# Performance work log

Hardware: AMD Instinct MI355X
Metric: run time of the kernel (lower is better)

## Reference

```python
import jax, jax.numpy as jnp
import numpy as np

N, C, H, W = 64, 512, 32, 32
HID, NCLS = 240, 10


def setup_inputs() -> dict:
    key = jax.random.key(0)
    ks = jax.random.split(key, 6)
    d = {
        "x": jax.random.normal(ks[0], (N, C, H, W), jnp.float32),
        "bn1_g": jnp.ones((C,), jnp.float32),
        "bn1_b": jnp.zeros((C,), jnp.float32),
        "bn1_m": jnp.zeros((C,), jnp.float32),
        "bn1_v": jnp.ones((C,), jnp.float32),
        "conv1_w": jax.random.normal(ks[1], (C, C, 3, 3), jnp.float32) * 0.02,
        "bn2_g": jnp.ones((C,), jnp.float32),
        "bn2_b": jnp.zeros((C,), jnp.float32),
        "bn2_m": jnp.zeros((C,), jnp.float32),
        "bn2_v": jnp.ones((C,), jnp.float32),
        "conv2_w": jax.random.normal(ks[2], (C, C, 3, 3), jnp.float32) * 0.02,
        "fc1_w": jax.random.normal(ks[3], (HID, C), jnp.float32) * 0.05,
        "fc1_b": jnp.zeros((HID,), jnp.float32),
        "fc2_w": jax.random.normal(ks[4], (NCLS, HID), jnp.float32) * 0.05,
        "fc2_b": jnp.zeros((NCLS,), jnp.float32),
    }
    return d


def _bn(x, g, b, m, v, eps=1e-5):
    # eval-mode BatchNorm2d, NCHW
    inv = g / jnp.sqrt(v + eps)
    return x * inv[None, :, None, None] + (b - m * inv)[None, :, None, None]


def _conv3(x, w):
    return jax.lax.conv_general_dilated(
        x, w, window_strides=(1, 1), padding="SAME",
        dimension_numbers=("NCHW", "OIHW", "NCHW"))


def _probe(feat, fc1_w, fc1_b, fc2_w, fc2_b):
    # Global_Avg_Flatten -> Linear -> Softplus(beta=5) -> Linear
    g = feat.mean(axis=(2, 3))                       # (N, C)
    h = jax.nn.softplus(5.0 * (g @ fc1_w.T + fc1_b)) / 5.0  # (N, HID)
    return h @ fc2_w.T + fc2_b                       # (N, NCLS)


def _get_mask(feat, fc1_w, fc1_b, fc2_w, fc2_b):
    # eval branch: sum of top-1 + top-2 logits, grad wrt (detached) feat
    feat_sg = jax.lax.stop_gradient(feat)

    def logit_sum(f_):
        logits = _probe(f_, fc1_w, fc1_b, fc2_w, fc2_b)
        idx = jax.lax.top_k(logits, 2)[1]            # (N, 2) int indices
        return jnp.take_along_axis(logits, idx, axis=1).sum()

    g = jax.grad(logit_sum)(feat_sg)                 # (N, C, H, W)
    # adaptive_avg_pool2d(.,1)*H*W == spatial sum
    s = g.sum(axis=(2, 3))                           # (N, C)
    m = jax.nn.softmax(s, axis=1) * 2.0
    return m[:, :, None, None]


def reference(x, bn1_g, bn1_b, bn1_m, bn1_v, conv1_w,
              bn2_g, bn2_b, bn2_m, bn2_v, conv2_w,
              fc1_w, fc1_b, fc2_w, fc2_b):
    out1 = jax.nn.relu(_bn(x, bn1_g, bn1_b, bn1_m, bn1_v))  # equalInOut path
    mask = _get_mask(out1, fc1_w, fc1_b, fc2_w, fc2_b)
    pred_probe = _probe(out1, fc1_w, fc1_b, fc2_w, fc2_b)
    masked = out1 * mask
    h = jax.nn.relu(_bn(_conv3(masked, conv1_w), bn2_g, bn2_b, bn2_m, bn2_v))
    h = _conv3(h, conv2_w)
    out = x + h
    return (out, pred_probe)
```

## Files before the change

kernel.cpp:

```cpp
#include <hip/hip_runtime.h>
#include <stdint.h>

typedef __bf16 bf16x8 __attribute__((ext_vector_type(8)));
typedef float f32x4v __attribute__((ext_vector_type(4)));

typedef __attribute__((address_space(1))) const void gconst_t;
typedef __attribute__((address_space(3))) void lds_t;

#define GLL16(gp, sp) __builtin_amdgcn_global_load_lds((gconst_t*)(uintptr_t)(gp), (lds_t*)(uintptr_t)(sp), 16, 0, 0)

__device__ __forceinline__ unsigned short f2bf(float f) {
  unsigned int u = __float_as_uint(f);
  u = (u + 0x7FFFu + ((u >> 16) & 1u)) >> 16;
  return (unsigned short)u;
}
__device__ __forceinline__ float bf2f(unsigned int b) {
  return __uint_as_float(b << 16);
}

#define SPP 1156

__global__ __launch_bounds__(512) void bnprep(
    const float* __restrict__ g1, const float* __restrict__ b1,
    const float* __restrict__ m1, const float* __restrict__ v1,
    const float* __restrict__ g2, const float* __restrict__ b2,
    const float* __restrict__ m2, const float* __restrict__ v2,
    float* __restrict__ bnp) {
  int t = threadIdx.x;
  float i1 = g1[t] * rsqrtf(v1[t] + 1e-5f);
  bnp[t] = i1;
  bnp[512 + t] = b1[t] - m1[t] * i1;
  float i2 = g2[t] * rsqrtf(v2[t] + 1e-5f);
  bnp[1024 + t] = i2;
  bnp[1536 + t] = b2[t] - m2[t] * i2;
}

__global__ __launch_bounds__(256) void wtrans(const float* __restrict__ w1, const float* __restrict__ w2,
                                              unsigned short* __restrict__ w1t, unsigned short* __restrict__ w2t) {
  unsigned e = blockIdx.x * 256u + threadIdx.x;
  if (e >= 4718592u) return;
  const float* w = (e < 2359296u) ? w1 : w2;
  unsigned short* o = (e < 2359296u) ? w1t : w2t;
  unsigned r = (e < 2359296u) ? e : (e - 2359296u);
  unsigned ci = r & 511u, co = (r >> 9) & 511u, tt = r >> 18;
  o[r] = f2bf(w[(co * 512u + ci) * 9u + tt]);
}

__global__ __launch_bounds__(256) void bn1_relu_stage(const float* __restrict__ x, const float* __restrict__ bnp,
                                                      unsigned short* __restrict__ Ap, float* __restrict__ partial) {
  int bid = blockIdx.x;
  int n = bid >> 6, ciblk = (bid >> 3) & 7, yblk = bid & 7;
  int ci0 = ciblk * 64, y0 = yblk * 4;
  int t = threadIdx.x;
  __shared__ __align__(16) float vals[64 * 128];
  __shared__ float ivs[64], bbs[64];
  if (t < 64) { ivs[t] = bnp[ci0 + t]; bbs[t] = bnp[512 + ci0 + t]; }
  __syncthreads();
#pragma unroll
  for (int i = 0; i < 8; ++i) {
    int f4 = i * 256 + t;
    int cil = f4 >> 5, xq = f4 & 31;
    const float* src = x + ((size_t)(n * 512 + ci0 + cil)) * 1024 + y0 * 32 + xq * 4;
    f32x4v v = *(const f32x4v*)src;
    float iv = ivs[cil], bb = bbs[cil];
    f32x4v r;
    r[0] = fmaxf(fmaf(v[0], iv, bb), 0.f);
    r[1] = fmaxf(fmaf(v[1], iv, bb), 0.f);
    r[2] = fmaxf(fmaf(v[2], iv, bb), 0.f);
    r[3] = fmaxf(fmaf(v[3], iv, bb), 0.f);
    *(f32x4v*)&vals[cil * 128 + xq * 4] = r;
  }
  __syncthreads();
  {
    int cil = t >> 2, q = t & 3;
    float s = 0.f;
#pragma unroll
    for (int j = 0; j < 32; ++j) s += vals[cil * 128 + q * 32 + j];
    s += __shfl_xor(s, 1);
    s += __shfl_xor(s, 2);
    if (q == 0) partial[((size_t)n * 512 + ci0 + cil) * 8 + yblk] = s;
  }
  {
    int yx = t >> 1, half = t & 1;
    int y = y0 + (yx >> 5), xx = yx & 31;
    unsigned short* dp = Ap + ((size_t)((n * 34 + y + 1) * 34 + (xx + 1))) * 512 + ci0 + half * 32;
    unsigned wrd[16];
#pragma unroll
    for (int j = 0; j < 16; ++j) {
      unsigned lo = f2bf(vals[(half * 32 + 2 * j) * 128 + yx]);
      unsigned hi = f2bf(vals[(half * 32 + 2 * j + 1) * 128 + yx]);
      wrd[j] = lo | (hi << 16);
    }
#pragma unroll
    for (int k = 0; k < 4; ++k) {
      uint4 u;
      u.x = wrd[k * 4]; u.y = wrd[k * 4 + 1]; u.z = wrd[k * 4 + 2]; u.w = wrd[k * 4 + 3];
      *(uint4*)(dp + k * 8) = u;
    }
  }
}

__global__ __launch_bounds__(256) void probe_mask(const float* __restrict__ partial,
                                                  const float* __restrict__ fc1w, const float* __restrict__ fc1b,
                                                  const float* __restrict__ fc2w, const float* __restrict__ fc2b,
                                                  float* __restrict__ maskp, float* __restrict__ probeout) {
  int n = blockIdx.x, t = threadIdx.x;
  int lane = t & 63, wv = t >> 6;
  __shared__ float gl[512], sl[512], zl[240], hl[240], dzl[240], logl[10], red[4];
  __shared__ int idx2[2];
  for (int c = t; c < 512; c += 256) {
    const float* pp = partial + ((size_t)n * 512 + c) * 8;
    float s = 0.f;
#pragma unroll
    for (int j = 0; j < 8; ++j) s += pp[j];
    gl[c] = s * (1.f / 1024.f);
  }
  __syncthreads();
  if (t < 240) {
    float z = fc1b[t];
    const float* wr = fc1w + t * 512;
    for (int c = 0; c < 512; ++c) z = fmaf(gl[c], wr[c], z);
    zl[t] = z;
    float u = 5.f * z;
    float sp = (u > 20.f) ? u : log1pf(expf(u));
    hl[t] = sp * 0.2f;
  }
  __syncthreads();
  if (t < 10) {
    float L = fc2b[t];
    const float* wr = fc2w + t * 240;
    for (int h = 0; h < 240; ++h) L = fmaf(hl[h], wr[h], L);
    logl[t] = L;
    probeout[n * 10 + t] = L;
  }
  __syncthreads();
  if (t == 0) {
    float b1v = -1e30f, b2v = -1e30f; int i1 = 0, i2 = 0;
    for (int j = 0; j < 10; ++j) {
      float v = logl[j];
      if (v > b1v) { b2v = b1v; i2 = i1; b1v = v; i1 = j; }
      else if (v > b2v) { b2v = v; i2 = j; }
    }
    idx2[0] = i1; idx2[1] = i2;
  }
  __syncthreads();
  if (t < 240) {
    float dh = fc2w[idx2[0] * 240 + t] + fc2w[idx2[1] * 240 + t];
    float u = 5.f * zl[t];
    float sg = 1.f / (1.f + expf(-u));
    dzl[t] = dh * sg;
  }
  __syncthreads();
  for (int c = t; c < 512; c += 256) {
    float s = 0.f;
    for (int h = 0; h < 240; ++h) s = fmaf(dzl[h], fc1w[h * 512 + c], s);
    sl[c] = s;
  }
  __syncthreads();
  float m = fmaxf(sl[t], sl[t + 256]);
#pragma unroll
  for (int o = 32; o > 0; o >>= 1) m = fmaxf(m, __shfl_xor(m, o));
  if (lane == 0) red[wv] = m;
  __syncthreads();
  float mx = fmaxf(fmaxf(red[0], red[1]), fmaxf(red[2], red[3]));
  float e0 = expf(sl[t] - mx), e1 = expf(sl[t + 256] - mx);
  float sum = e0 + e1;
#pragma unroll
  for (int o = 32; o > 0; o >>= 1) sum += __shfl_xor(sum, o);
  __syncthreads();
  if (lane == 0) red[wv] = sum;
  __syncthreads();
  float inv = 2.f / (red[0] + red[1] + red[2] + red[3]);
  maskp[(size_t)n * 512 + t] = e0 * inv;
  maskp[(size_t)n * 512 + t + 256] = e1 * inv;
}

__global__ __launch_bounds__(256) void apply_mask(unsigned short* __restrict__ Ap, const float* __restrict__ maskp) {
  int n = blockIdx.y;
  size_t off = (size_t)n * (SPP * 512) + (size_t)blockIdx.x * 2048 + threadIdx.x * 8;
  int ci0 = (int)(threadIdx.x * 8) & 511;
  uint4 v = *(uint4*)(Ap + off);
  const float* mp = maskp + n * 512 + ci0;
  unsigned r0, r1;
  r0 = f2bf(bf2f(v.x & 0xFFFFu) * mp[0]); r1 = f2bf(bf2f(v.x >> 16) * mp[1]); v.x = r0 | (r1 << 16);
  r0 = f2bf(bf2f(v.y & 0xFFFFu) * mp[2]); r1 = f2bf(bf2f(v.y >> 16) * mp[3]); v.y = r0 | (r1 << 16);
  r0 = f2bf(bf2f(v.z & 0xFFFFu) * mp[4]); r1 = f2bf(bf2f(v.z >> 16) * mp[5]); v.z = r0 | (r1 << 16);
  r0 = f2bf(bf2f(v.w & 0xFFFFu) * mp[6]); r1 = f2bf(bf2f(v.w >> 16) * mp[7]); v.w = r0 | (r1 << 16);
  *(uint4*)(Ap + off) = v;
}

#define RD_A(QM, BOF) do {                                                    \
  const char* _p = ldsb + (BOF) + aRd + (QM) * 8192;                          \
  _Pragma("unroll") for (int mi = 0; mi < 4; ++mi) {                          \
    a[mi][0] = *(const bf16x8*)(_p + mi * 2048);                              \
    a[mi][1] = *(const bf16x8*)(_p + mi * 2048 + 64); }                       \
} while (0)

#define RD_B(QN, BOF) do {                                                    \
  const char* _p = ldsb + (BOF) + bRd + (QN) * 4096;                          \
  _Pragma("unroll") for (int ni = 0; ni < 2; ++ni) {                          \
    b[QN][ni][0] = *(const bf16x8*)(_p + ni * 2048);                          \
    b[QN][ni][1] = *(const bf16x8*)(_p + ni * 2048 + 64); }                   \
} while (0)

#define ST_A(BOF, H, AP) do {                                                 \
  GLL16((AP) + aOff[H][0], ldsb + (BOF) + (H) * 16384 + tb);                  \
  GLL16((AP) + aOff[H][1], ldsb + (BOF) + (H) * 16384 + 8192 + tb);           \
} while (0)

#define ST_B(BOF, H, BP) do {                                                 \
  GLL16((BP) + bOff[H][0], ldsb + 65536 + (BOF) + (H) * 16384 + tb);          \
  GLL16((BP) + bOff[H][1], ldsb + 65536 + (BOF) + (H) * 16384 + 8192 + tb);   \
} while (0)

#define MFMA_Q(QM, QN) do {                                                   \
  _Pragma("unroll") for (int mi = 0; mi < 4; ++mi)                            \
  _Pragma("unroll") for (int ni = 0; ni < 2; ++ni) {                          \
    acc[QM][QN][mi][ni] = __builtin_amdgcn_mfma_f32_16x16x32_bf16(            \
        a[mi][0], b[QN][ni][0], acc[QM][QN][mi][ni], 0, 0, 0);                \
    acc[QM][QN][mi][ni] = __builtin_amdgcn_mfma_f32_16x16x32_bf16(            \
        a[mi][1], b[QN][ni][1], acc[QM][QN][mi][ni], 0, 0, 0); }              \
} while (0)

#define BARR __builtin_amdgcn_s_barrier()
#define LGKM0 do { asm volatile("s_waitcnt lgkmcnt(0)" ::: "memory");         \
                   __builtin_amdgcn_sched_barrier(0); } while (0)
#define VM4 asm volatile("s_waitcnt vmcnt(4)" ::: "memory")
#define PRIO1 __builtin_amdgcn_s_setprio(1)
#define PRIO0 __builtin_amdgcn_s_setprio(0)

#define TILE_PTRS(KT, APn, BPn)                                               \
  const unsigned short *APn, *BPn;                                            \
  { int _kt = (KT); int _tap = _kt >> 3; int _kin = (_kt & 7) << 6;           \
    int _dy = (_tap * 11) >> 5; int _dx = _tap - _dy * 3;                     \
    APn = Ag + (size_t)(_dy * 34 + _dx) * 512 + _kin;                         \
    BPn = Wt + (size_t)_tap * 262144 + _kin; }

template <int MODE>
__global__ __launch_bounds__(512, 2) void conv256(
    const unsigned short* __restrict__ Ain,
    const unsigned short* __restrict__ Wt,
    const float* __restrict__ bnp,
    unsigned short* __restrict__ Hout,
    const float* __restrict__ xres,
    float* __restrict__ outp) {
  __shared__ __align__(16) char ldsb[131072];

  const int t = threadIdx.x;
  const int lane = t & 63;
  const int wv = t >> 6;
  const int wm = wv >> 2;
  const int wn = wv & 3;

  const int bid = blockIdx.x;
  const int swz = (bid & 7) * 64 + (bid >> 3);
  const int nt = swz & 1, mt = swz >> 1;
  const int n = mt >> 2, yblk = mt & 3;
  const int co0 = nt * 256;

  const unsigned short* Ag = Ain + (size_t)n * (SPP * 512);

  int aOff[2][2], bOff[2][2];
#pragma unroll
  for (int i = 0; i < 2; ++i) {
    const int c = i * 512 + t;
    const int lr = c >> 3;
    const int kq = (c & 7) ^ ((lr >> 1) & 2);
#pragma unroll
    for (int h = 0; h < 2; ++h) {
      aOff[h][i] = ((yblk * 8 + h * 4 + (lr >> 5)) * 34 + (lr & 31)) * 512 + kq * 8;
      bOff[h][i] = (co0 + h * 128 + lr) * 512 + kq * 8;
    }
  }
  const int tb = t * 16;
  const int kterm = ((lane >> 4) << 4) ^ ((lane & 4) << 3);
  const int aRd = wm * 16384 + (lane & 15) * 128 + kterm;
  const int bRd = 65536 + (wn >> 1) * 16384 + (((wn & 1) << 6) + (lane & 15)) * 128 + kterm;

  bf16x8 a[4][2];
  bf16x8 b[2][2][2];
  f32x4v acc[2][2][4][2];
  const f32x4v zero = {0.f, 0.f, 0.f, 0.f};
#pragma unroll
  for (int qm = 0; qm < 2; ++qm)
#pragma unroll
    for (int qn = 0; qn < 2; ++qn)
#pragma unroll
      for (int mi = 0; mi < 4; ++mi)
#pragma unroll
        for (int ni = 0; ni < 2; ++ni) acc[qm][qn][mi][ni] = zero;

  {
    TILE_PTRS(0, ap0, bp0);
    TILE_PTRS(1, ap1p, bp1p);
    ST_B(0, 0, bp0); ST_B(0, 1, bp0);
    ST_A(0, 0, ap0); ST_A(0, 1, ap0);
    ST_B(32768, 0, bp1p); ST_B(32768, 1, bp1p);
    (void)ap1p;
    VM4;
    BARR;
  }

  for (int it = 0; it < 36; ++it) {
    const int u = 2 * it;
    TILE_PTRS(u + 1, ap1, bp1);
    (void)bp1;
    int kt2 = u + 2; if (kt2 > 71) kt2 = 71;
    int kt3 = u + 3; if (kt3 > 71) kt3 = 71;
    TILE_PTRS(kt2, ap2, bp2);
    TILE_PTRS(kt3, ap3, bp3);
    (void)ap3;

    RD_A(0, 0); RD_B(0, 0);
    ST_A(32768, 0, ap1);
    BARR; LGKM0;
    PRIO1; MFMA_Q(0, 0); PRIO0;
    BARR;
    RD_B(1, 0);
    ST_A(32768, 1, ap1);
    BARR; LGKM0;
    PRIO1; MFMA_Q(0, 1); PRIO0;
    BARR;
    RD_A(1, 0);
    ST_B(0, 0, bp2);
    BARR; LGKM0;
    PRIO1; MFMA_Q(1, 1); PRIO0;
    BARR;
    ST_B(0, 1, bp2);
    BARR;
    PRIO1; MFMA_Q(1, 0); PRIO0;
    VM4;
    BARR;
    RD_A(0, 32768); RD_B(0, 32768);
    ST_A(0, 0, ap2);
    BARR; LGKM0;
    PRIO1; MFMA_Q(0, 0); PRIO0;
    BARR;
    RD_B(1, 32768);
    ST_A(0, 1, ap2);
    BARR; LGKM0;
    PRIO1; MFMA_Q(0, 1); PRIO0;
    BARR;
    RD_A(1, 32768);
    ST_B(32768, 0, bp3);
    BARR; LGKM0;
    PRIO1; MFMA_Q(1, 1); PRIO0;
    BARR;
    ST_B(32768, 1, bp3);
    BARR;
    PRIO1; MFMA_Q(1, 0); PRIO0;
    VM4;
    BARR;
  }
  asm volatile("s_waitcnt vmcnt(0)" ::: "memory");
  __syncthreads();

  if constexpr (MODE == 1) {
#pragma unroll
    for (int qn = 0; qn < 2; ++qn)
#pragma unroll
      for (int ni = 0; ni < 2; ++ni) {
        const int cog = co0 + wn * 64 + qn * 32 + ni * 16 + (lane & 15);
        const float iv = bnp[1024 + cog];
        const float bb = bnp[1536 + cog];
#pragma unroll
        for (int qm = 0; qm < 2; ++qm)
#pragma unroll
          for (int mi = 0; mi < 4; ++mi)
#pragma unroll
            for (int r = 0; r < 4; ++r) {
              const int row = wm * 128 + qm * 64 + mi * 16 + (lane >> 4) * 4 + r;
              const int y = yblk * 8 + (row >> 5), xx = row & 31;
              const float v = fmaxf(fmaf(acc[qm][qn][mi][ni][r], iv, bb), 0.f);
              Hout[((size_t)((n * 34 + y + 1) * 34 + (xx + 1))) * 512 + cog] = f2bf(v);
            }
      }
  } else {
    float* sm = (float*)ldsb;
    const int spat0 = yblk * 256;
#pragma unroll 1
    for (int h = 0; h < 4; ++h) {
      if (wn == h) {
#pragma unroll
        for (int qn = 0; qn < 2; ++qn)
#pragma unroll
          for (int ni = 0; ni < 2; ++ni)
#pragma unroll
            for (int qm = 0; qm < 2; ++qm)
#pragma unroll
              for (int mi = 0; mi < 4; ++mi)
#pragma unroll
                for (int r = 0; r < 4; ++r)
                  sm[(qn * 32 + ni * 16 + (lane & 15)) * 264 +
                     wm * 128 + qm * 64 + mi * 16 + (lane >> 4) * 4 + r] = acc[qm][qn][mi][ni][r];
      }
      __syncthreads();
#pragma unroll
      for (int j = 0; j < 8; ++j) {
        const int c = j * 512 + t;
        const int cc = c >> 6, px = (c & 63) * 4;
        f32x4v v = *(const f32x4v*)&sm[cc * 264 + px];
        const int cog = co0 + h * 64 + cc;
        const size_t o = ((size_t)(n * 512 + cog)) * 1024 + spat0 + px;
        const f32x4v xr = *(const f32x4v*)(xres + o);
        v = v + xr;
        *(f32x4v*)(outp + o) = v;
      }
      __syncthreads();
    }
  }
}

extern "C" void kernel_launch(void* const* d_in, const int* in_sizes, int n_in,
                              void* d_out, int out_size, void* d_ws, size_t ws_size,
                              hipStream_t stream) {
  (void)in_sizes; (void)n_in; (void)out_size; (void)ws_size;
  const float* x    = (const float*)d_in[0];
  const float* bn1g = (const float*)d_in[1];
  const float* bn1b = (const float*)d_in[2];
  const float* bn1m = (const float*)d_in[3];
  const float* bn1v = (const float*)d_in[4];
  const float* w1   = (const float*)d_in[5];
  const float* bn2g = (const float*)d_in[6];
  const float* bn2b = (const float*)d_in[7];
  const float* bn2m = (const float*)d_in[8];
  const float* bn2v = (const float*)d_in[9];
  const float* w2   = (const float*)d_in[10];
  const float* fc1w = (const float*)d_in[11];
  const float* fc1b = (const float*)d_in[12];
  const float* fc2w = (const float*)d_in[13];
  const float* fc2b = (const float*)d_in[14];

  float* out = (float*)d_out;
  float* probeo = out + (size_t)64 * 512 * 32 * 32;

  char* ws = (char*)d_ws;
  unsigned short* Ap  = (unsigned short*)(ws);
  unsigned short* Hp  = (unsigned short*)(ws + 75759616);
  unsigned short* W1t = (unsigned short*)(ws + 151519232);
  unsigned short* W2t = (unsigned short*)(ws + 156237824);
  float* partial      = (float*)(ws + 160956416);
  float* maskp        = (float*)(ws + 162004992);
  float* bnp          = (float*)(ws + 162136064);

  hipMemsetAsync(Ap, 0, 75759616, stream);
  hipMemsetAsync(Hp, 0, 75759616, stream);
  bnprep<<<1, 512, 0, stream>>>(bn1g, bn1b, bn1m, bn1v, bn2g, bn2b, bn2m, bn2v, bnp);
  wtrans<<<18432, 256, 0, stream>>>(w1, w2, W1t, W2t);
  bn1_relu_stage<<<4096, 256, 0, stream>>>(x, bnp, Ap, partial);
  probe_mask<<<64, 256, 0, stream>>>(partial, fc1w, fc1b, fc2w, fc2b, maskp, probeo);
  apply_mask<<<dim3(289, 64), 256, 0, stream>>>(Ap, maskp);
  conv256<1><<<512, 512, 0, stream>>>(Ap, W1t, bnp, Hp, nullptr, nullptr);
  conv256<2><<<512, 512, 0, stream>>>(Hp, W2t, bnp, nullptr, x, out);
}
```

Baseline: 684.6 us.

## Zero only padding ring instead of full buffers; use full XOR LDS swizzle

Replaces two full-buffer memsets of the padded activation buffers with a small kernel that zeroes only the one-pixel border ring, since interiors are fully overwritten later. This removes roughly 150 MB of write traffic per call. It also changes the LDS k-chunk swizzle from a 2-bit to a full 3-bit XOR of row index, with matching read offsets, to reduce LDS bank conflicts in the conv GEMM. The ring-only zeroing depends on every interior element being written by the producer kernels.

Measured after the change: 616.3 us. -10.0%, faster.

```diff
diff --git a/kernel.cpp b/kernel.cpp
--- a/kernel.cpp
+++ b/kernel.cpp
@@ -35,6 +35,22 @@
   bnp[1536 + t] = b2[t] - m2[t] * i2;
 }
 
+__global__ __launch_bounds__(256) void ring_zero(unsigned short* __restrict__ Ap,
+                                                 unsigned short* __restrict__ Hp) {
+  const int n = blockIdx.y;
+  const int p = blockIdx.x * 4 + (threadIdx.x >> 6);
+  const int lane = threadIdx.x & 63;
+  int y, x;
+  if (p < 34) { y = 0; x = p; }
+  else if (p < 68) { y = 33; x = p - 34; }
+  else if (p < 100) { y = p - 67; x = 0; }
+  else { y = p - 99; x = 33; }
+  const uint4 z = {0u, 0u, 0u, 0u};
+  const size_t off = ((size_t)((n * 34 + y) * 34 + x)) * 512 + lane * 8;
+  *(uint4*)(Ap + off) = z;
+  *(uint4*)(Hp + off) = z;
+}
+
 __global__ __launch_bounds__(256) void wtrans(const float* __restrict__ w1, const float* __restrict__ w2,
                                               unsigned short* __restrict__ w1t, unsigned short* __restrict__ w2t) {
   unsigned e = blockIdx.x * 256u + threadIdx.x;
@@ -190,17 +206,19 @@
 }
 
 #define RD_A(QM, BOF) do {                                                    \
-  const char* _p = ldsb + (BOF) + aRd + (QM) * 8192;                          \
+  const char* _p0 = ldsb + (BOF) + (QM) * 8192 + aRd0;                        \
+  const char* _p1 = ldsb + (BOF) + (QM) * 8192 + aRd1;                        \
   _Pragma("unroll") for (int mi = 0; mi < 4; ++mi) {                          \
-    a[mi][0] = *(const bf16x8*)(_p + mi * 2048);                              \
-    a[mi][1] = *(const bf16x8*)(_p + mi * 2048 + 64); }                       \
+    a[mi][0] = *(const bf16x8*)(_p0 + mi * 2048);                             \
+    a[mi][1] = *(const bf16x8*)(_p1 + mi * 2048); }                           \
 } while (0)
 
 #define RD_B(QN, BOF) do {                                                    \
-  const char* _p = ldsb + (BOF) + bRd + (QN) * 4096;                          \
+  const char* _p0 = ldsb + (BOF) + (QN) * 4096 + bRd0;                        \
+  const char* _p1 = ldsb + (BOF) + (QN) * 4096 + bRd1;                        \
   _Pragma("unroll") for (int ni = 0; ni < 2; ++ni) {                          \
-    b[QN][ni][0] = *(const bf16x8*)(_p + ni * 2048);                          \
-    b[QN][ni][1] = *(const bf16x8*)(_p + ni * 2048 + 64); }                   \
+    b[QN][ni][0] = *(const bf16x8*)(_p0 + ni * 2048);                         \
+    b[QN][ni][1] = *(const bf16x8*)(_p1 + ni * 2048); }                       \
 } while (0)
 
 #define ST_A(BOF, H, AP) do {                                                 \
@@ -265,7 +283,7 @@
   for (int i = 0; i < 2; ++i) {
     const int c = i * 512 + t;
     const int lr = c >> 3;
-    const int kq = (c & 7) ^ ((lr >> 1) & 2);
+    const int kq = (c & 7) ^ (lr & 7);
 #pragma unroll
     for (int h = 0; h < 2; ++h) {
       aOff[h][i] = ((yblk * 8 + h * 4 + (lr >> 5)) * 34 + (lr & 31)) * 512 + kq * 8;
@@ -273,9 +291,11 @@
     }
   }
   const int tb = t * 16;
-  const int kterm = ((lane >> 4) << 4) ^ ((lane & 4) << 3);
-  const int aRd = wm * 16384 + (lane & 15) * 128 + kterm;
-  const int bRd = 65536 + (wn >> 1) * 16384 + (((wn & 1) << 6) + (lane & 15)) * 128 + kterm;
+  const int k0 = (((lane >> 4) ^ (lane & 7)) << 4);
+  const int aRd0 = wm * 16384 + (lane & 15) * 128 + k0;
+  const int aRd1 = aRd0 ^ 64;
+  const int bRd0 = 65536 + (wn >> 1) * 16384 + (((wn & 1) << 6) + (lane & 15)) * 128 + k0;
+  const int bRd1 = bRd0 ^ 64;
 
   bf16x8 a[4][2];
   bf16x8 b[2][2][2];
@@ -443,9 +463,8 @@
   float* maskp        = (float*)(ws + 162004992);
   float* bnp          = (float*)(ws + 162136064);
 
-  hipMemsetAsync(Ap, 0, 75759616, stream);
-  hipMemsetAsync(Hp, 0, 75759616, stream);
   bnprep<<<1, 512, 0, stream>>>(bn1g, bn1b, bn1m, bn1v, bn2g, bn2b, bn2m, bn2v, bnp);
+  ring_zero<<<dim3(33, 64), 256, 0, stream>>>(Ap, Hp);
   wtrans<<<18432, 256, 0, stream>>>(w1, w2, W1t, W2t);
   bn1_relu_stage<<<4096, 256, 0, stream>>>(x, bnp, Ap, partial);
   probe_mask<<<64, 256, 0, stream>>>(partial, fc1w, fc1b, fc2w, fc2b, maskp, probeo);
```
